# Optimization experiments

Measured on AMD Instinct MI355X. Metric: run time of the kernel, lower is better.

Reference implementation:

```python
import jax, jax.numpy as jnp
import numpy as np

BITS = 4
PACK = 32 // BITS          # 8 int4 values per int32
GROUP_SIZE = 128
ZERO_POINT = 8             # uint4b8: symmetric quant, implicit zp = 8


def _dequantize(qweight, scales):
    """Unpack GPTQ column-packed int4 weights and dequantize.

    qweight: [K // 8, N] int32, 8 nibbles per int32 along K.
    scales:  [K // GROUP_SIZE, N] float.
    Returns W: [K, N] float32 where W[k, n] = (nib - 8) * scales[k // 128, n].
    """
    Kp, N = qweight.shape
    shifts = (BITS * jnp.arange(PACK, dtype=jnp.int32))[None, :, None]   # [1,8,1]
    nibbles = jax.lax.shift_right_logical(qweight[:, None, :], shifts) & 0xF  # [K/8,8,N]
    w_int = nibbles.reshape(Kp * PACK, N)                                 # [K,N]
    w = w_int.astype(jnp.float32) - float(ZERO_POINT)
    # desc_act=False -> g_idx is identity, groups are contiguous blocks of 128 rows
    return w * jnp.repeat(scales.astype(jnp.float32), GROUP_SIZE, axis=0)


def setup_inputs() -> dict:
    key = jax.random.key(0)
    k1, k2, k3 = jax.random.split(key, 3)
    M, K, N = 8192, 4096, 4096
    x = jax.random.normal(k1, (M, K), dtype=jnp.float32)
    qweight = jax.random.randint(k2, (K // PACK, N), 0, 2147483647, dtype=jnp.int32)
    # small positive per-group scales, as produced by GPTQ calibration
    scales = jax.random.uniform(k3, (K // GROUP_SIZE, N), dtype=jnp.float32) * 0.01 + 0.001
    return {"x": x, "qweight": qweight, "scales": scales}


def reference(x, qweight, scales):
    # Equivalent math to apply_gptq_marlin_linear with sym int4, no bias,
    # no act_order (identity g_idx), fp32 reduction.
    w = _dequantize(qweight, scales)          # [K, N]
    return jnp.matmul(x, w)                   # [M, N]
```

## Files before the change

kernel.cpp:

```cpp
#include <hip/hip_runtime.h>
#include <hip/hip_bf16.h>
#include <stdint.h>


#define M_DIM 8192
#define K_DIM 4096
#define N_DIM 4096

#define BM 128
#define BN 128
#define BK 64

typedef __attribute__((ext_vector_type(8))) short s16x8;
typedef __attribute__((ext_vector_type(8))) unsigned short u16x8;
typedef __attribute__((ext_vector_type(4))) float f32x4;
typedef unsigned int u32;

#define AS1 __attribute__((address_space(1)))
#define AS3 __attribute__((address_space(3)))

__device__ __forceinline__ void gload_lds16(const void* g, void* l) {
    __builtin_amdgcn_global_load_lds((const AS1 u32*)g, (AS3 u32*)l, 16, 0, 0);
}

__device__ __forceinline__ unsigned short f32_to_bf16_rne(float f) {
    union { float f; u32 u; } v; v.f = f;
    u32 u = v.u;
    u32 r = (u + 0x7FFFu + ((u >> 16) & 1u)) >> 16;
    return (unsigned short)r;
}

__global__ __launch_bounds__(256) void cvt_x_bf16(const float* __restrict__ in,
                                                  unsigned short* __restrict__ out) {
    const int i = blockIdx.x * 256 + threadIdx.x;
    const f32x4* p = (const f32x4*)in + (size_t)i * 2;
    f32x4 a = p[0], b = p[1];
    u16x8 r;
    r[0] = f32_to_bf16_rne(a[0]); r[1] = f32_to_bf16_rne(a[1]);
    r[2] = f32_to_bf16_rne(a[2]); r[3] = f32_to_bf16_rne(a[3]);
    r[4] = f32_to_bf16_rne(b[0]); r[5] = f32_to_bf16_rne(b[1]);
    r[6] = f32_to_bf16_rne(b[2]); r[7] = f32_to_bf16_rne(b[3]);
    ((u16x8*)out)[i] = r;
}

__global__ __launch_bounds__(256) void dequant_wt(const int* __restrict__ qw,
                                                  const float* __restrict__ scales,
                                                  unsigned short* __restrict__ wt) {
    const int bid = blockIdx.x;
    const int nb  = (bid & (N_DIM / 16 - 1)) * 16;
    const int kpb = (bid >> 8) * 16;
    const int tid = threadIdx.x;
    const int n   = nb + ((tid >> 6) << 2) + (tid & 3);
    const int kp  = kpb + ((tid >> 2) & 15);
    const u32 q = ((const u32*)qw)[(size_t)kp * N_DIM + n];
    const float s = scales[(size_t)(kp >> 4) * N_DIM + n];
    u16x8 r;
#pragma unroll
    for (int j = 0; j < 8; j++) {
        const int w = (int)((q >> (4 * j)) & 0xFu) - 8;
        r[j] = f32_to_bf16_rne((float)w * s);
    }
    *(u16x8*)(&wt[(size_t)n * K_DIM + (size_t)kp * 8]) = r;
}

__global__ __launch_bounds__(256) void gemm_bf16_bt(const unsigned short* __restrict__ A,
                                                    const unsigned short* __restrict__ Bt,
                                                    float* __restrict__ C) {
    __shared__ unsigned short As[BM * BK];
    __shared__ unsigned short Bs[BN * BK];

    const int tid  = threadIdx.x;
    const int wave = tid >> 6;
    const int lane = tid & 63;

    const int nwg = gridDim.x;
    const int cpx = nwg >> 3;
    const int bid = blockIdx.x;
    const int wg  = (bid & 7) * cpx + (bid >> 3);

    const int nbn = N_DIM / BN;
    const int m0 = (wg / nbn) * BM;
    const int n0 = (wg % nbn) * BN;

    const int wm = wave >> 1;
    const int wn = wave & 1;

    const int srow = lane >> 3;
    const int scol = ((lane & 7) ^ (lane >> 3)) * 8;
    const unsigned short* gA = A  + (size_t)(m0 + wave * 32 + srow) * K_DIM + scol;
    const unsigned short* gB = Bt + (size_t)(n0 + wave * 32 + srow) * K_DIM + scol;

    const int fr = lane & 15;
    const int fq = lane >> 4;
    const int r7 = fr & 7;
    const unsigned short* lA = &As[(size_t)(wm * 64 + fr) * BK];
    const unsigned short* lB = &Bs[(size_t)(wn * 64 + fr) * BK];

    f32x4 acc[4][4] = {};

    for (int k0 = 0; k0 < K_DIM; k0 += BK) {
#pragma unroll
        for (int i = 0; i < 4; i++) {
            gload_lds16(gA + (size_t)i * 8 * K_DIM + k0, &As[(wave * 4 + i) * 512]);
            gload_lds16(gB + (size_t)i * 8 * K_DIM + k0, &Bs[(wave * 4 + i) * 512]);
        }
        __syncthreads();
#pragma unroll
        for (int kk = 0; kk < BK; kk += 32) {
            const int kko = kk >> 3;
            s16x8 af[4], bfr[4];
#pragma unroll
            for (int m = 0; m < 4; m++)
                af[m]  = *(const s16x8*)(lA + m * 16 * BK + (((fq + kko) ^ r7) << 3));
#pragma unroll
            for (int n = 0; n < 4; n++)
                bfr[n] = *(const s16x8*)(lB + n * 16 * BK + (((fq + kko) ^ r7) << 3));
#pragma unroll
            for (int m = 0; m < 4; m++)
#pragma unroll
                for (int n = 0; n < 4; n++)
                    acc[m][n] = __builtin_amdgcn_mfma_f32_16x16x32_bf16(
                        af[m], bfr[n], acc[m][n], 0, 0, 0);
        }
        __syncthreads();
    }

#pragma unroll
    for (int m = 0; m < 4; m++) {
        const int row = m0 + wm * 64 + m * 16 + fq * 4;
#pragma unroll
        for (int n = 0; n < 4; n++) {
            const int col = n0 + wn * 64 + n * 16 + fr;
            float* cp = C + (size_t)row * N_DIM + col;
#pragma unroll
            for (int r = 0; r < 4; r++) cp[(size_t)r * N_DIM] = acc[m][n][r];
        }
    }
}

extern "C" void kernel_launch(void* const* d_in, const int* in_sizes, int n_in,
                              void* d_out, int out_size, void* d_ws, size_t ws_size,
                              hipStream_t stream) {
    const float* x  = (const float*)d_in[0];
    const int*   qw = (const int*)d_in[1];
    const float* sc = (const float*)d_in[2];
    float* out = (float*)d_out;

    unsigned short* xbf = (unsigned short*)d_ws;
    unsigned short* wt  = (unsigned short*)((char*)d_ws + (size_t)M_DIM * K_DIM * 2);

    cvt_x_bf16<<<(M_DIM * (size_t)K_DIM) / 8 / 256, 256, 0, stream>>>(x, xbf);
    dequant_wt<<<(K_DIM / 8 / 16) * (N_DIM / 16), 256, 0, stream>>>(qw, sc, wt);
    gemm_bf16_bt<<<(M_DIM / BM) * (N_DIM / BN), 256, 0, stream>>>(xbf, wt, out);
}
```

Before: 524.8 us.

## Replace GEMM with 256x256-tile, 8-wave, multi-buffered 8-phase pipelined kernel

```diff
diff --git a/kernel.cpp b/kernel.cpp
--- a/kernel.cpp
+++ b/kernel.cpp
@@ -6,10 +6,6 @@
 #define M_DIM 8192
 #define K_DIM 4096
 #define N_DIM 4096
-
-#define BM 128
-#define BN 128
-#define BK 64
 
 typedef __attribute__((ext_vector_type(8))) short s16x8;
 typedef __attribute__((ext_vector_type(8))) unsigned short u16x8;
@@ -63,79 +59,112 @@
     *(u16x8*)(&wt[(size_t)n * K_DIM + (size_t)kp * 8]) = r;
 }
 
-__global__ __launch_bounds__(256) void gemm_bf16_bt(const unsigned short* __restrict__ A,
-                                                    const unsigned short* __restrict__ Bt,
-                                                    float* __restrict__ C) {
-    __shared__ unsigned short As[BM * BK];
-    __shared__ unsigned short Bs[BN * BK];
+
+#define DS_A(BUF,KH,MH,mm) (*(const s16x8*)(pA + (BUF)*16384 + (KH)*8192 + (MH)*2048 + (mm)*512))
+#define DS_B(BUF,KH,n)     (*(const s16x8*)(pB + (BUF)*16384 + (KH)*8192 + (n)*512))
+
+#define STAGE4(BUF,KH,GK) do { int gk_ = (GK); if (gk_ > K_DIM - 32) gk_ = K_DIM - 32; \
+    gload_lds16(gA0 + gk_, ldsA + ((BUF)*2+(KH))*8192 + dstL);                          \
+    gload_lds16(gA1 + gk_, ldsA + ((BUF)*2+(KH))*8192 + dstH);                          \
+    gload_lds16(gB0 + gk_, ldsB + ((BUF)*2+(KH))*8192 + dstL);                          \
+    gload_lds16(gB1 + gk_, ldsB + ((BUF)*2+(KH))*8192 + dstH); } while (0)
+
+#define MROW(MH,mm,AREG)                                                                      \
+    acc[(MH)*4+(mm)][0] = __builtin_amdgcn_mfma_f32_16x16x32_bf16(AREG, bf0, acc[(MH)*4+(mm)][0], 0, 0, 0); \
+    acc[(MH)*4+(mm)][1] = __builtin_amdgcn_mfma_f32_16x16x32_bf16(AREG, bf1, acc[(MH)*4+(mm)][1], 0, 0, 0); \
+    acc[(MH)*4+(mm)][2] = __builtin_amdgcn_mfma_f32_16x16x32_bf16(AREG, bf2, acc[(MH)*4+(mm)][2], 0, 0, 0); \
+    acc[(MH)*4+(mm)][3] = __builtin_amdgcn_mfma_f32_16x16x32_bf16(AREG, bf3, acc[(MH)*4+(mm)][3], 0, 0, 0);
+
+#define NOOP ((void)0)
+
+#define PHASE(BUF,KH,MH,LOADB,STAGE_STMT,TAIL_STMT)              \
+    {                                                            \
+        if (LOADB) {                                             \
+            bf0 = DS_B(BUF,KH,0); bf1 = DS_B(BUF,KH,1);          \
+            bf2 = DS_B(BUF,KH,2); bf3 = DS_B(BUF,KH,3);          \
+        }                                                        \
+        a0 = DS_A(BUF,KH,MH,0); a1 = DS_A(BUF,KH,MH,1);          \
+        a2 = DS_A(BUF,KH,MH,2); a3 = DS_A(BUF,KH,MH,3);          \
+        STAGE_STMT;                                              \
+        __builtin_amdgcn_s_barrier();                            \
+        asm volatile("s_waitcnt lgkmcnt(0)" ::: "memory");       \
+        __builtin_amdgcn_sched_barrier(0);                       \
+        __builtin_amdgcn_s_setprio(1);                           \
+        MROW(MH,0,a0) MROW(MH,1,a1) MROW(MH,2,a2) MROW(MH,3,a3)  \
+        __builtin_amdgcn_s_setprio(0);                           \
+        TAIL_STMT;                                               \
+        __builtin_amdgcn_s_barrier();                            \
+    }
+
+#define VMC4 asm volatile("s_waitcnt vmcnt(4)" ::: "memory")
+
+__global__ __launch_bounds__(512, 2) void gemm_bf16_8ph(const unsigned short* __restrict__ A,
+                                                        const unsigned short* __restrict__ Bt,
+                                                        float* __restrict__ C) {
+    __shared__ unsigned short As[2 * 2 * 8192];
+    __shared__ unsigned short Bs[2 * 2 * 8192];
 
     const int tid  = threadIdx.x;
     const int wave = tid >> 6;
     const int lane = tid & 63;
 
-    const int nwg = gridDim.x;
-    const int cpx = nwg >> 3;
     const int bid = blockIdx.x;
-    const int wg  = (bid & 7) * cpx + (bid >> 3);
+    const int wg  = (bid & 7) * (512 / 8) + (bid >> 3);
+    const int m0 = (wg >> 4) * 256;
+    const int n0 = (wg & 15) * 256;
 
-    const int nbn = N_DIM / BN;
-    const int m0 = (wg / nbn) * BM;
-    const int n0 = (wg % nbn) * BN;
+    const int wr = wave >> 2;
+    const int wc = wave & 3;
 
-    const int wm = wave >> 1;
-    const int wn = wave & 1;
-
-    const int srow = lane >> 3;
-    const int scol = ((lane & 7) ^ (lane >> 3)) * 8;
-    const unsigned short* gA = A  + (size_t)(m0 + wave * 32 + srow) * K_DIM + scol;
-    const unsigned short* gB = Bt + (size_t)(n0 + wave * 32 + srow) * K_DIM + scol;
+    unsigned short* ldsA = &As[0];
+    unsigned short* ldsB = &Bs[0];
+    const int dstL = wave * 512;
+    const int dstH = 4096 + wave * 512;
+    const unsigned short* gA0 = A  + (size_t)(m0 + wave * 16 + (lane >> 2)) * K_DIM + (lane & 3) * 8;
+    const unsigned short* gA1 = gA0 + (size_t)128 * K_DIM;
+    const unsigned short* gB0 = Bt + (size_t)(n0 + wave * 16 + (lane >> 2)) * K_DIM + (lane & 3) * 8;
+    const unsigned short* gB1 = gB0 + (size_t)128 * K_DIM;
 
     const int fr = lane & 15;
     const int fq = lane >> 4;
-    const int r7 = fr & 7;
-    const unsigned short* lA = &As[(size_t)(wm * 64 + fr) * BK];
-    const unsigned short* lB = &Bs[(size_t)(wn * 64 + fr) * BK];
+    const unsigned short* pA = ldsA + (wr * 128 + fr) * 32 + fq * 8;
+    const unsigned short* pB = ldsB + (wc * 64 + fr) * 32 + fq * 8;
 
-    f32x4 acc[4][4] = {};
+    f32x4 acc[8][4] = {};
+    s16x8 a0, a1, a2, a3, bf0, bf1, bf2, bf3;
 
-    for (int k0 = 0; k0 < K_DIM; k0 += BK) {
-#pragma unroll
-        for (int i = 0; i < 4; i++) {
-            gload_lds16(gA + (size_t)i * 8 * K_DIM + k0, &As[(wave * 4 + i) * 512]);
-            gload_lds16(gB + (size_t)i * 8 * K_DIM + k0, &Bs[(wave * 4 + i) * 512]);
-        }
-        __syncthreads();
-#pragma unroll
-        for (int kk = 0; kk < BK; kk += 32) {
-            const int kko = kk >> 3;
-            s16x8 af[4], bfr[4];
-#pragma unroll
-            for (int m = 0; m < 4; m++)
-                af[m]  = *(const s16x8*)(lA + m * 16 * BK + (((fq + kko) ^ r7) << 3));
-#pragma unroll
-            for (int n = 0; n < 4; n++)
-                bfr[n] = *(const s16x8*)(lB + n * 16 * BK + (((fq + kko) ^ r7) << 3));
-#pragma unroll
-            for (int m = 0; m < 4; m++)
-#pragma unroll
-                for (int n = 0; n < 4; n++)
-                    acc[m][n] = __builtin_amdgcn_mfma_f32_16x16x32_bf16(
-                        af[m], bfr[n], acc[m][n], 0, 0, 0);
-        }
-        __syncthreads();
+    STAGE4(0, 0, 0);
+    STAGE4(0, 1, 32);
+    STAGE4(1, 0, 64);
+    VMC4;
+    __builtin_amdgcn_s_barrier();
+
+    for (int kb = 0; kb < K_DIM; kb += 128) {
+        PHASE(0, 0, 0, 1, STAGE4(1, 1, kb + 96),  NOOP);
+        PHASE(0, 0, 1, 0, NOOP,                   NOOP);
+        PHASE(0, 1, 0, 1, STAGE4(0, 0, kb + 128), NOOP);
+        PHASE(0, 1, 1, 0, NOOP,                   VMC4);
+        PHASE(1, 0, 0, 1, STAGE4(0, 1, kb + 160), NOOP);
+        PHASE(1, 0, 1, 0, NOOP,                   NOOP);
+        PHASE(1, 1, 0, 1, STAGE4(1, 0, kb + 192), NOOP);
+        PHASE(1, 1, 1, 0, NOOP,                   VMC4);
     }
 
+    asm volatile("s_waitcnt vmcnt(0)" ::: "memory");
+
 #pragma unroll
-    for (int m = 0; m < 4; m++) {
-        const int row = m0 + wm * 64 + m * 16 + fq * 4;
+    for (int mh = 0; mh < 2; mh++)
 #pragma unroll
-        for (int n = 0; n < 4; n++) {
-            const int col = n0 + wn * 64 + n * 16 + fr;
-            float* cp = C + (size_t)row * N_DIM + col;
+        for (int mm = 0; mm < 4; mm++) {
+            const int row = m0 + wr * 128 + mh * 64 + mm * 16 + fq * 4;
 #pragma unroll
-            for (int r = 0; r < 4; r++) cp[(size_t)r * N_DIM] = acc[m][n][r];
+            for (int n = 0; n < 4; n++) {
+                const int col = n0 + wc * 64 + n * 16 + fr;
+                float* cp = C + (size_t)row * N_DIM + col;
+#pragma unroll
+                for (int r = 0; r < 4; r++) cp[(size_t)r * N_DIM] = acc[mh * 4 + mm][n][r];
+            }
         }
-    }
 }
 
 extern "C" void kernel_launch(void* const* d_in, const int* in_sizes, int n_in,
@@ -151,5 +180,5 @@
 
     cvt_x_bf16<<<(M_DIM * (size_t)K_DIM) / 8 / 256, 256, 0, stream>>>(x, xbf);
     dequant_wt<<<(K_DIM / 8 / 16) * (N_DIM / 16), 256, 0, stream>>>(qw, sc, wt);
-    gemm_bf16_bt<<<(M_DIM / BM) * (N_DIM / BN), 256, 0, stream>>>(xbf, wt, out);
+    gemm_bf16_8ph<<<(M_DIM / 256) * (N_DIM / 256), 512, 0, stream>>>(xbf, wt, out);
 }
```

After: 501.9 us. -4.3%, faster.

## Rewrite GEMM as 256x256 tile with multi-stage LDS pipeline and register double-buffering

Applied to the files above, without the earlier changes.

```diff
diff --git a/kernel.cpp b/kernel.cpp
--- a/kernel.cpp
+++ b/kernel.cpp
@@ -6,10 +6,6 @@
 #define M_DIM 8192
 #define K_DIM 4096
 #define N_DIM 4096
-
-#define BM 128
-#define BN 128
-#define BK 64
 
 typedef __attribute__((ext_vector_type(8))) short s16x8;
 typedef __attribute__((ext_vector_type(8))) unsigned short u16x8;
@@ -63,74 +59,118 @@
     *(u16x8*)(&wt[(size_t)n * K_DIM + (size_t)kp * 8]) = r;
 }
 
-__global__ __launch_bounds__(256) void gemm_bf16_bt(const unsigned short* __restrict__ A,
-                                                    const unsigned short* __restrict__ Bt,
-                                                    float* __restrict__ C) {
-    __shared__ unsigned short As[BM * BK];
-    __shared__ unsigned short Bs[BN * BK];
+__device__ __forceinline__ void loadf(s16x8 (&a)[8], s16x8 (&b)[8],
+                                      const unsigned short* pA,
+                                      const unsigned short* pB, int reg_off) {
+#pragma unroll
+    for (int i = 0; i < 8; i++) {
+        a[i] = *(const s16x8*)(pA + reg_off + i * 512);
+        b[i] = *(const s16x8*)(pB + reg_off + i * 512);
+    }
+}
+
+__device__ __forceinline__ void mfma64(const s16x8 (&a)[8], const s16x8 (&b)[8],
+                                       f32x4 (&acc)[8][8]) {
+#pragma unroll
+    for (int m = 0; m < 8; m++)
+#pragma unroll
+        for (int n = 0; n < 8; n++)
+            acc[m][n] = __builtin_amdgcn_mfma_f32_16x16x32_bf16(a[m], b[n], acc[m][n], 0, 0, 0);
+}
+
+#define R00 0
+#define R01 8192
+#define R10 16384
+#define R11 24576
+
+#define STAGE8(BUF,KH,GK) do { int gk_ = (GK); if (gk_ > K_DIM - 32) gk_ = K_DIM - 32; \
+    const int ro_ = ((BUF)*2+(KH))*8192 + wave*512;                                    \
+    _Pragma("unroll")                                                                  \
+    for (int j_ = 0; j_ < 4; j_++) {                                                   \
+        gload_lds16(gA0 + (size_t)(j_*64)*K_DIM + gk_, ldsA + ro_ + j_*2048);          \
+        gload_lds16(gB0 + (size_t)(j_*64)*K_DIM + gk_, ldsB + ro_ + j_*2048);          \
+    } } while (0)
+
+#define BARR()  __builtin_amdgcn_s_barrier()
+#define LGKM0() do { asm volatile("s_waitcnt lgkmcnt(0)" ::: "memory"); \
+                     __builtin_amdgcn_sched_barrier(0); } while (0)
+#define SBAR()  __builtin_amdgcn_sched_barrier(0)
+#define VMC8    asm volatile("s_waitcnt vmcnt(8)" ::: "memory")
+#define VMC0    asm volatile("s_waitcnt vmcnt(0)" ::: "memory")
+
+__global__ __launch_bounds__(256, 1) void gemm_bf16_4w(const unsigned short* __restrict__ A,
+                                                       const unsigned short* __restrict__ Bt,
+                                                       float* __restrict__ C) {
+    __shared__ unsigned short As[2 * 2 * 8192];
+    __shared__ unsigned short Bs[2 * 2 * 8192];
 
     const int tid  = threadIdx.x;
     const int wave = tid >> 6;
     const int lane = tid & 63;
 
-    const int nwg = gridDim.x;
-    const int cpx = nwg >> 3;
     const int bid = blockIdx.x;
-    const int wg  = (bid & 7) * cpx + (bid >> 3);
+    const int wg  = (bid & 7) * (512 / 8) + (bid >> 3);
+    const int m0 = (wg >> 4) * 256;
+    const int n0 = (wg & 15) * 256;
 
-    const int nbn = N_DIM / BN;
-    const int m0 = (wg / nbn) * BM;
-    const int n0 = (wg % nbn) * BN;
+    const int wr = wave >> 1;
+    const int wc = wave & 1;
 
-    const int wm = wave >> 1;
-    const int wn = wave & 1;
-
-    const int srow = lane >> 3;
-    const int scol = ((lane & 7) ^ (lane >> 3)) * 8;
-    const unsigned short* gA = A  + (size_t)(m0 + wave * 32 + srow) * K_DIM + scol;
-    const unsigned short* gB = Bt + (size_t)(n0 + wave * 32 + srow) * K_DIM + scol;
+    unsigned short* ldsA = &As[0];
+    unsigned short* ldsB = &Bs[0];
+    const int srow  = tid >> 2;
+    const int scol8 = ((tid & 3) ^ (srow & 3)) * 8;
+    const unsigned short* gA0 = A  + (size_t)(m0 + srow) * K_DIM + scol8;
+    const unsigned short* gB0 = Bt + (size_t)(n0 + srow) * K_DIM + scol8;
 
     const int fr = lane & 15;
     const int fq = lane >> 4;
-    const int r7 = fr & 7;
-    const unsigned short* lA = &As[(size_t)(wm * 64 + fr) * BK];
-    const unsigned short* lB = &Bs[(size_t)(wn * 64 + fr) * BK];
+    const unsigned short* pA = ldsA + (wr * 128 + fr) * 32 + ((fq ^ (fr & 3)) << 3);
+    const unsigned short* pB = ldsB + (wc * 128 + fr) * 32 + ((fq ^ (fr & 3)) << 3);
 
-    f32x4 acc[4][4] = {};
+    f32x4 acc[8][8] = {};
+    s16x8 aR[8], bR[8], aS[8], bS[8];
 
-    for (int k0 = 0; k0 < K_DIM; k0 += BK) {
-#pragma unroll
-        for (int i = 0; i < 4; i++) {
-            gload_lds16(gA + (size_t)i * 8 * K_DIM + k0, &As[(wave * 4 + i) * 512]);
-            gload_lds16(gB + (size_t)i * 8 * K_DIM + k0, &Bs[(wave * 4 + i) * 512]);
-        }
-        __syncthreads();
-#pragma unroll
-        for (int kk = 0; kk < BK; kk += 32) {
-            const int kko = kk >> 3;
-            s16x8 af[4], bfr[4];
-#pragma unroll
-            for (int m = 0; m < 4; m++)
-                af[m]  = *(const s16x8*)(lA + m * 16 * BK + (((fq + kko) ^ r7) << 3));
-#pragma unroll
-            for (int n = 0; n < 4; n++)
-                bfr[n] = *(const s16x8*)(lB + n * 16 * BK + (((fq + kko) ^ r7) << 3));
-#pragma unroll
-            for (int m = 0; m < 4; m++)
-#pragma unroll
-                for (int n = 0; n < 4; n++)
-                    acc[m][n] = __builtin_amdgcn_mfma_f32_16x16x32_bf16(
-                        af[m], bfr[n], acc[m][n], 0, 0, 0);
-        }
-        __syncthreads();
+    STAGE8(0, 0, 0);
+    STAGE8(0, 1, 32);
+    STAGE8(1, 0, 64);
+    VMC8;
+    BARR();
+    loadf(aR, bR, pA, pB, R00);
+
+    for (int kb = 0; kb < K_DIM; kb += 128) {
+        STAGE8(1, 1, kb + 96);
+        BARR(); LGKM0();
+        __builtin_amdgcn_s_setprio(1); mfma64(aR, bR, acc); __builtin_amdgcn_s_setprio(0);
+        loadf(aS, bS, pA, pB, R01); SBAR();
+        BARR();
+        STAGE8(0, 0, kb + 128);
+        BARR(); LGKM0();
+        __builtin_amdgcn_s_setprio(1); mfma64(aS, bS, acc); __builtin_amdgcn_s_setprio(0);
+        VMC8;
+        loadf(aR, bR, pA, pB, R10); SBAR();
+        BARR();
+        STAGE8(0, 1, kb + 160);
+        BARR(); LGKM0();
+        __builtin_amdgcn_s_setprio(1); mfma64(aR, bR, acc); __builtin_amdgcn_s_setprio(0);
+        loadf(aS, bS, pA, pB, R11); SBAR();
+        BARR();
+        STAGE8(1, 0, kb + 192);
+        BARR(); LGKM0();
+        __builtin_amdgcn_s_setprio(1); mfma64(aS, bS, acc); __builtin_amdgcn_s_setprio(0);
+        VMC8;
+        loadf(aR, bR, pA, pB, R00); SBAR();
+        BARR();
     }
 
+    VMC0;
+
 #pragma unroll
-    for (int m = 0; m < 4; m++) {
-        const int row = m0 + wm * 64 + m * 16 + fq * 4;
+    for (int m = 0; m < 8; m++) {
+        const int row = m0 + wr * 128 + m * 16 + fq * 4;
 #pragma unroll
-        for (int n = 0; n < 4; n++) {
-            const int col = n0 + wn * 64 + n * 16 + fr;
+        for (int n = 0; n < 8; n++) {
+            const int col = n0 + wc * 128 + n * 16 + fr;
             float* cp = C + (size_t)row * N_DIM + col;
 #pragma unroll
             for (int r = 0; r < 4; r++) cp[(size_t)r * N_DIM] = acc[m][n][r];
@@ -151,5 +191,5 @@
 
     cvt_x_bf16<<<(M_DIM * (size_t)K_DIM) / 8 / 256, 256, 0, stream>>>(x, xbf);
     dequant_wt<<<(K_DIM / 8 / 16) * (N_DIM / 16), 256, 0, stream>>>(qw, sc, wt);
-    gemm_bf16_bt<<<(M_DIM / BM) * (N_DIM / BN), 256, 0, stream>>>(xbf, wt, out);
+    gemm_bf16_4w<<<(M_DIM / 256) * (N_DIM / 256), 256, 0, stream>>>(xbf, wt, out);
 }
```

After: 476.5 us. -9.2%, faster.
